# Optimization experiments

Hardware: AMD Instinct MI355X
Metric: run time of the kernel (lower is better)

Reference implementation:

```python
import jax, jax.numpy as jnp
import numpy as np

H = 256       # hidden_dim
LAT = 8       # latent_dim
NC = 8        # num_edge_classes
B = 65536     # batch of edge decisions
EPS = 1e-5    # LayerNorm eps (torch default)


def _ln(x, g, b):
    m = jnp.mean(x, axis=-1, keepdims=True)
    v = jnp.var(x, axis=-1, keepdims=True)
    return (x - m) * jax.lax.rsqrt(v + EPS) * g + b


def setup_inputs() -> dict:
    key = jax.random.key(0)
    ks = jax.random.split(key, 32)
    rn = lambda k, shape: (jax.random.normal(k, shape, dtype=jnp.float32) * 0.02)
    inp = {
        "node_i": jax.random.normal(ks[0], (B, H), dtype=jnp.float32),
        "node_j": jax.random.normal(ks[1], (B, H), dtype=jnp.float32),
        "latent": jax.random.normal(ks[2], (B, LAT), dtype=jnp.float32),
        "edge_hidden_state": jax.random.normal(ks[3], (B, H), dtype=jnp.float32),
        "previous_edge_token": jax.random.randint(ks[4], (B,), 0, NC, dtype=jnp.int32),
        # edge_encoder: Linear(2H->H) + LayerNorm
        "We": rn(ks[5], (2 * H, H)), "be": jnp.zeros((H,), jnp.float32),
        "ge": jnp.ones((H,), jnp.float32), "bee": jnp.zeros((H,), jnp.float32),
        # context_proj: Linear(LAT->H)
        "Wc": rn(ks[6], (LAT, H)), "bc": jnp.zeros((H,), jnp.float32),
        # MultiheadAttention in/out projections (q,k mathematically inert: kv_len=1)
        "Wq": rn(ks[7], (H, H)), "bq": jnp.zeros((H,), jnp.float32),
        "Wk": rn(ks[8], (H, H)), "bk": jnp.zeros((H,), jnp.float32),
        "Wv": rn(ks[9], (H, H)), "bv": jnp.zeros((H,), jnp.float32),
        "Wo": rn(ks[10], (H, H)), "bo": jnp.zeros((H,), jnp.float32),
        # post-attention LayerNorm
        "gn": jnp.ones((H,), jnp.float32), "bn": jnp.zeros((H,), jnp.float32),
        # edge token embedding [NC, H]
        "emb": rn(ks[11], (NC, H)),
        # GRUCell(2H -> H): gates packed as [r|z|n] along output dim (torch order)
        "W_ih": rn(ks[12], (2 * H, 3 * H)), "b_ih": jnp.zeros((3 * H,), jnp.float32),
        "W_hh": rn(ks[13], (H, 3 * H)), "b_hh": jnp.zeros((3 * H,), jnp.float32),
        # fusion: Linear(3H->H) + LayerNorm
        "Wf": rn(ks[14], (3 * H, H)), "bf": jnp.zeros((H,), jnp.float32),
        "gf": jnp.ones((H,), jnp.float32), "bff": jnp.zeros((H,), jnp.float32),
        # output head: Linear(H->H//2) + ReLU + Linear(H//2->NC)
        "W1": rn(ks[15], (H, H // 2)), "b1": jnp.zeros((H // 2,), jnp.float32),
        "W2": rn(ks[16], (H // 2, NC)), "b2": jnp.zeros((NC,), jnp.float32),
    }
    return inp


def _forward(node_i, node_j, latent, edge_hidden_state, previous_edge_token,
             We, be, ge, bee, Wc, bc, Wq, bq, Wk, bk, Wv, bv, Wo, bo,
             gn, bn, emb, W_ih, b_ih, W_hh, b_hh, Wf, bf, gf, bff,
             W1, b1, W2, b2):
    # edge encoder (eval mode: dropout is identity)
    edge = jax.nn.relu(_ln(jnp.concatenate([node_i, node_j], axis=-1) @ We + be, ge, bee))
    # context projection [B, H] (seq_len 1, squeezed)
    context = latent @ Wc + bc
    # cross-attention with a single key/value: softmax over one key == 1 exactly,
    # so attended = out_proj(value_proj(context)); q/k projections cancel out.
    v = context @ Wv + bv
    attended = _ln(v @ Wo + bo, gn, bn)
    prev_embed = emb[previous_edge_token]                      # [B, H]
    x = jnp.concatenate([attended, prev_embed], axis=-1)       # [B, 2H]
    gi = x @ W_ih + b_ih                                       # [B, 3H]
    gh = edge_hidden_state @ W_hh + b_hh                       # [B, 3H]
    r = jax.nn.sigmoid(gi[:, :H] + gh[:, :H])
    z = jax.nn.sigmoid(gi[:, H:2 * H] + gh[:, H:2 * H])
    n = jnp.tanh(gi[:, 2 * H:] + r * gh[:, 2 * H:])
    new_h = (1.0 - z) * n + z * edge_hidden_state
    fused = jax.nn.relu(_ln(jnp.concatenate([edge, attended, new_h], axis=-1) @ Wf + bf, gf, bff))
    logits = jax.nn.relu(fused @ W1 + b1) @ W2 + b2            # [B, NC]
    return logits, new_h


def reference(node_i, node_j, latent, edge_hidden_state, previous_edge_token,
              We, be, ge, bee, Wc, bc, Wq, bq, Wk, bk, Wv, bv, Wo, bo,
              gn, bn, emb, W_ih, b_ih, W_hh, b_hh, Wf, bf, gf, bff,
              W1, b1, W2, b2):
    return _forward(node_i, node_j, latent, edge_hidden_state, previous_edge_token,
                    We, be, ge, bee, Wc, bc, Wq, bq, Wk, bk, Wv, bv, Wo, bo,
                    gn, bn, emb, W_ih, b_ih, W_hh, b_hh, Wf, bf, gf, bff,
                    W1, b1, W2, b2)
```

## Files before the change

kernel.cpp:

```cpp
#include <hip/hip_runtime.h>


typedef __bf16 bf16;
typedef _Float16 f16;
typedef __attribute__((ext_vector_type(8))) _Float16 f16x8;
typedef __attribute__((ext_vector_type(4))) float f32x4;

#define HD 256
#define RPB 64
#define AST 260
#define AST2 264
#define TPB 1024
#define TPM 512

#define FB_OFF 65536
#define WE_E 0
#define WIH_E 131072
#define WHH_E 327680
#define WF_E 524288
#define W1_E 720896
#define FRAG_ELEMS 753664
#define WS_NEED (FB_OFF + FRAG_ELEMS * 2)

__device__ __forceinline__ float bf2f(unsigned short u) {
  union { unsigned int i; float f; } c; c.i = ((unsigned)u) << 16; return c.f;
}
__device__ __forceinline__ float4 ld4c(const float* p) { return *(const float4*)p; }
__device__ __forceinline__ float4 ld4c(const bf16* p) {
  ushort4 u = *(const ushort4*)p;
  return make_float4(bf2f(u.x), bf2f(u.y), bf2f(u.z), bf2f(u.w));
}
template <class T>
__device__ __forceinline__ float ld(const T* __restrict__ p) { return (float)*p; }

__device__ __forceinline__ f32x4 MFMA16(f16x8 a, f16x8 b, f32x4 c) {
  return __builtin_amdgcn_mfma_f32_16x16x32_f16(a, b, c, 0, 0, 0);
}

__global__ void k_detect(const unsigned int* __restrict__ wds, int* __restrict__ flag, int nw) {
  __shared__ int sRed[4];
  int t = threadIdx.x;
  int cnt = 0;
  for (int i = t; i < nw; i += 256) {
    unsigned e = (wds[i] >> 7) & 0xFFu;
    cnt += (e >= 110u && e <= 140u) ? 1 : 0;
  }
#pragma unroll
  for (int m = 1; m < 64; m <<= 1) cnt += __shfl_xor(cnt, m);
  if ((t & 63) == 0) sRed[t >> 6] = cnt;
  __syncthreads();
  if (t == 0) flag[0] = (sRed[0] + sRed[1] + sRed[2] + sRed[3] > nw / 2) ? 1 : 0;
}

template <class T, int WANT>
__global__ void k_cvo_a(const int* __restrict__ flag, const T* __restrict__ Wc,
                        const T* __restrict__ Wv, const T* __restrict__ bc,
                        const T* __restrict__ bv, float* __restrict__ tmp) {
  if (*flag != WANT) return;
  int i = blockIdx.x;
  int m = threadIdx.x;
  float s = 0.f;
  if (i < 8) {
    for (int u = 0; u < 256; ++u) s += ld(Wc + i * 256 + u) * ld(Wv + (size_t)u * 256 + m);
  } else {
    for (int u = 0; u < 256; ++u) s += ld(bc + u) * ld(Wv + (size_t)u * 256 + m);
    s += ld(bv + m);
  }
  tmp[i * 256 + m] = s;
}

template <class T, int WANT>
__global__ void k_cvo_b(const int* __restrict__ flag, const float* __restrict__ tmp,
                        const T* __restrict__ Wo, const T* __restrict__ bo,
                        float* __restrict__ Wcvo, float* __restrict__ bcvo) {
  if (*flag != WANT) return;
  int i = blockIdx.x;
  int m = threadIdx.x;
  float s = 0.f;
  const float* tr = tmp + i * 256;
  for (int u = 0; u < 256; ++u) s += tr[u] * ld(Wo + (size_t)u * 256 + m);
  if (i < 8) Wcvo[i * 256 + m] = s;
  else       bcvo[m] = s + ld(bo + m);
}

__global__ void k_prep(const int* __restrict__ flag,
                       const float* We, const float* Wih, const float* Whh,
                       const float* Wf, const float* W1, f16* __restrict__ dst) {
  if (*flag != 0) return;
  const float* srcs[5] = {We, Wih, Whh, Wf, W1};
  const int Ns[5] = {256, 768, 768, 256, 128};
  const int offs[6] = {WE_E, WIH_E, WHH_E, WF_E, W1_E, FRAG_ELEMS};
  int t = blockIdx.x * blockDim.x + threadIdx.x;
  int np = gridDim.x * blockDim.x;
  for (int seg = 0; seg < 5; ++seg) {
    const float* s = srcs[seg];
    int N = Ns[seg], NT = N >> 4;
    f16* d = dst + offs[seg];
    int n = offs[seg + 1] - offs[seg];
    for (int e = t; e < n; e += np) {
      int j = e & 7, lx = (e >> 3) & 63, tl = e >> 9;
      int kt = tl / NT, nt = tl - kt * NT;
      int sk = kt * 32 + ((lx >> 4) << 3) + j;
      int sn = nt * 16 + (lx & 15);
      d[e] = (f16)s[(size_t)sk * N + sn];
    }
  }
}

__global__ void k_egru(const int* __restrict__ flag, const float* __restrict__ emb,
                       const float* __restrict__ Wih, const float* __restrict__ b_ih,
                       float* __restrict__ E) {
  if (*flag != 0) return;
  int tok = blockIdx.x, c = threadIdx.x;
  float s = b_ih[c];
  for (int k = 0; k < 256; ++k)
    s += emb[tok * 256 + k] * Wih[(size_t)(256 + k) * 768 + c];
  E[tok * 768 + c] = s;
}

__device__ __forceinline__ void mm4(f32x4 acc[2][4], const f16* __restrict__ X,
                                    int rowBase, int ktA0, int nKt,
                                    const f16* __restrict__ WB, int NT,
                                    int ktB0, int ntB, int lane16, int lg, int l) {
#pragma unroll 2
  for (int kt = 0; kt < nKt; ++kt) {
    const f16* xp = X + (size_t)(rowBase + lane16) * AST2 + (ktA0 + kt) * 32 + lg * 8;
    f16x8 a0 = *(const f16x8*)xp;
    f16x8 a1 = *(const f16x8*)(xp + 16 * AST2);
    const f16* wp = WB + (((size_t)(ktB0 + kt) * NT + ntB) * 64 + l) * 8;
#pragma unroll
    for (int nti = 0; nti < 4; ++nti) {
      f16x8 bfr = *(const f16x8*)(wp + nti * 512);
      acc[0][nti] = MFMA16(a0, bfr, acc[0][nti]);
      acc[1][nti] = MFMA16(a1, bfr, acc[1][nti]);
    }
  }
}

__device__ __forceinline__ void mm2(f32x4 acc[2][2], const f16* __restrict__ X,
                                    int rowBase, const f16* __restrict__ WB,
                                    int ntB, int lane16, int lg, int l) {
#pragma unroll 2
  for (int kt = 0; kt < 8; ++kt) {
    const f16* xp = X + (size_t)(rowBase + lane16) * AST2 + kt * 32 + lg * 8;
    f16x8 a0 = *(const f16x8*)xp;
    f16x8 a1 = *(const f16x8*)(xp + 16 * AST2);
    const f16* wp = WB + (((size_t)kt * 8 + ntB) * 64 + l) * 8;
#pragma unroll
    for (int nti = 0; nti < 2; ++nti) {
      f16x8 bfr = *(const f16x8*)(wp + nti * 512);
      acc[0][nti] = MFMA16(a0, bfr, acc[0][nti]);
      acc[1][nti] = MFMA16(a1, bfr, acc[1][nti]);
    }
  }
}

__device__ __forceinline__ void zero4(f32x4 acc[2][4]) {
#pragma unroll
  for (int a = 0; a < 2; ++a)
#pragma unroll
    for (int b = 0; b < 4; ++b) acc[a][b] = (f32x4){0.f, 0.f, 0.f, 0.f};
}

__device__ __forceinline__ void addB4(f32x4 acc[2][4], const float* bvec, int cg, int lane16) {
#pragma unroll
  for (int nti = 0; nti < 4; ++nti) {
    float bv = bvec[(cg * 4 + nti) * 16 + lane16];
#pragma unroll
    for (int rti = 0; rti < 2; ++rti)
#pragma unroll
      for (int r = 0; r < 4; ++r) acc[rti][nti][r] += bv;
  }
}

__device__ __forceinline__ void addE4(f32x4 acc[2][4], const float* __restrict__ E768,
                                      const int* __restrict__ tokS, int gateOff,
                                      int rtp, int cg, int lane16, int lg) {
#pragma unroll
  for (int rti = 0; rti < 2; ++rti)
#pragma unroll
    for (int r = 0; r < 4; ++r) {
      int grow = (rtp * 2 + rti) * 16 + lg * 4 + r;
      const float* er = E768 + tokS[grow] * 768 + gateOff;
#pragma unroll
      for (int nti = 0; nti < 4; ++nti)
        acc[rti][nti][r] += er[(cg * 4 + nti) * 16 + lane16];
    }
}

__device__ __forceinline__ void lnD(f32x4 acc[2][4], int rtp, int cg, int lane16, int lg,
                                    float* red, const float* g, const float* b, bool relu) {
  float sv[2][4], qv[2][4];
#pragma unroll
  for (int rti = 0; rti < 2; ++rti)
#pragma unroll
    for (int r = 0; r < 4; ++r) {
      float s = 0.f, q = 0.f;
#pragma unroll
      for (int nti = 0; nti < 4; ++nti) { float v = acc[rti][nti][r]; s += v; q += v * v; }
#pragma unroll
      for (int m = 1; m < 16; m <<= 1) { s += __shfl_xor(s, m); q += __shfl_xor(q, m); }
      sv[rti][r] = s; qv[rti][r] = q;
    }
  __syncthreads();
  if (lane16 == 0) {
#pragma unroll
    for (int rti = 0; rti < 2; ++rti)
#pragma unroll
      for (int r = 0; r < 4; ++r) {
        int grow = (rtp * 2 + rti) * 16 + lg * 4 + r;
        red[grow * 8 + cg * 2] = sv[rti][r];
        red[grow * 8 + cg * 2 + 1] = qv[rti][r];
      }
  }
  __syncthreads();
  float gv[4], bv[4];
#pragma unroll
  for (int nti = 0; nti < 4; ++nti) {
    int gc = (cg * 4 + nti) * 16 + lane16;
    gv[nti] = g[gc]; bv[nti] = b[gc];
  }
#pragma unroll
  for (int rti = 0; rti < 2; ++rti)
#pragma unroll
    for (int r = 0; r < 4; ++r) {
      int grow = (rtp * 2 + rti) * 16 + lg * 4 + r;
      float s = red[grow * 8 + 0] + red[grow * 8 + 2] + red[grow * 8 + 4] + red[grow * 8 + 6];
      float q = red[grow * 8 + 1] + red[grow * 8 + 3] + red[grow * 8 + 5] + red[grow * 8 + 7];
      float mean = s * (1.f / 256.f);
      float var = q * (1.f / 256.f) - mean * mean;
      float rstd = rsqrtf(var + 1e-5f);
#pragma unroll
      for (int nti = 0; nti < 4; ++nti) {
        float v = (acc[rti][nti][r] - mean) * rstd * gv[nti] + bv[nti];
        acc[rti][nti][r] = relu ? fmaxf(v, 0.f) : v;
      }
    }
}

__device__ __forceinline__ void scatD(f16* X, const f32x4 acc[2][4], int rtp, int cg,
                                      int lane16, int lg) {
#pragma unroll
  for (int rti = 0; rti < 2; ++rti)
#pragma unroll
    for (int r = 0; r < 4; ++r) {
      int grow = (rtp * 2 + rti) * 16 + lg * 4 + r;
#pragma unroll
      for (int nti = 0; nti < 4; ++nti) {
        int gc = (cg * 4 + nti) * 16 + lane16;
        X[(size_t)grow * AST2 + gc] = (f16)acc[rti][nti][r];
      }
    }
}

__device__ __forceinline__ void stageH(f16* dst, const float* __restrict__ src,
                                       int nv, int t) {
#pragma unroll
  for (int ii = 0; ii < 4; ++ii) {
    int i = t + ii * TPM;
    int r = i >> 5, c8 = i & 31;
    f16x8 h = (f16x8)(_Float16)0;
    if (r < nv) {
      const float* p = src + (size_t)r * HD + c8 * 8;
      float4 v0 = *(const float4*)p, v1 = *(const float4*)(p + 4);
      h[0] = (f16)v0.x; h[1] = (f16)v0.y; h[2] = (f16)v0.z; h[3] = (f16)v0.w;
      h[4] = (f16)v1.x; h[5] = (f16)v1.y; h[6] = (f16)v1.z; h[7] = (f16)v1.w;
    }
    *(f16x8*)(dst + (size_t)r * AST2 + c8 * 8) = h;
  }
}

__global__ __launch_bounds__(TPM, 4) void k_mfma(
    const int* __restrict__ flag, int Brows,
    const float* __restrict__ node_i, const float* __restrict__ node_j,
    const float* __restrict__ latent, const float* __restrict__ hin,
    const int* __restrict__ tok,
    const float* __restrict__ be, const float* __restrict__ ge, const float* __restrict__ bee,
    const float* __restrict__ gn, const float* __restrict__ bn,
    const float* __restrict__ b_hh,
    const float* __restrict__ bfb, const float* __restrict__ gf, const float* __restrict__ bff,
    const float* __restrict__ b1, const float* __restrict__ W2, const float* __restrict__ b2,
    const f16* __restrict__ WeF, const f16* __restrict__ WihF,
    const f16* __restrict__ WhhF, const f16* __restrict__ WfF,
    const f16* __restrict__ W1F,
    const float* __restrict__ Wcvo, const float* __restrict__ bcvo,
    const float* __restrict__ E768,
    float* __restrict__ outL, float* __restrict__ outNH) {
  if (*flag != 0) return;
  extern __shared__ char smc[];
  f16* X1 = (f16*)smc;
  f16* X2 = (f16*)(smc + 33792);
  float* red = (float*)(smc + 67584);
  float* sc  = (float*)(smc + 71680);
  int* tokS  = (int*)(smc + 73728);

  const int t = threadIdx.x;
  const int w = __builtin_amdgcn_readfirstlane(t >> 6);
  const int l = t & 63;
  const int lane16 = l & 15, lg = l >> 4;
  const int rtp = w & 1;
  const int cg = w >> 1;
  const int rowBase = rtp * 32;
  const int row0 = blockIdx.x * RPB;
  int nv = Brows - row0; if (nv > RPB) nv = RPB;

  if (t < 64) tokS[t] = (t < nv) ? tok[row0 + t] : 0;
  if (t < 512) sc[t] = ((t >> 3) < nv) ? latent[(size_t)row0 * 8 + t] : 0.f;
  stageH(X1, node_i + (size_t)row0 * HD, nv, t);
  __syncthreads();

  f32x4 acc[2][4];
  zero4(acc);
  mm4(acc, X1, rowBase, 0, 8, WeF, 16, 0, cg * 4, lane16, lg, l);
  __syncthreads();
  stageH(X1, node_j + (size_t)row0 * HD, nv, t);
  __syncthreads();
  mm4(acc, X1, rowBase, 0, 8, WeF, 16, 8, cg * 4, lane16, lg, l);
  addB4(acc, be, cg, lane16);
  lnD(acc, rtp, cg, lane16, lg, red, ge, bee, true);
  scatD(X2, acc, rtp, cg, lane16, lg);
  __syncthreads();

  f32x4 fac[2][4];
  zero4(fac);
  mm4(fac, X2, rowBase, 0, 8, WfF, 16, 0, cg * 4, lane16, lg, l);

  {
    float a32[32];
#pragma unroll
    for (int j4 = 0; j4 < 8; ++j4) {
      float4 v = *(const float4*)(bcvo + w * 32 + j4 * 4);
      a32[j4 * 4 + 0] = v.x; a32[j4 * 4 + 1] = v.y;
      a32[j4 * 4 + 2] = v.z; a32[j4 * 4 + 3] = v.w;
    }
#pragma unroll
    for (int k = 0; k < 8; ++k) {
      float xs = sc[l * 8 + k];
      const float* wr = Wcvo + k * 256 + w * 32;
#pragma unroll
      for (int j4 = 0; j4 < 8; ++j4) {
        float4 wv = *(const float4*)(wr + j4 * 4);
        a32[j4 * 4 + 0] = fmaf(xs, wv.x, a32[j4 * 4 + 0]);
        a32[j4 * 4 + 1] = fmaf(xs, wv.y, a32[j4 * 4 + 1]);
        a32[j4 * 4 + 2] = fmaf(xs, wv.z, a32[j4 * 4 + 2]);
        a32[j4 * 4 + 3] = fmaf(xs, wv.w, a32[j4 * 4 + 3]);
      }
    }
    float s = 0.f, q = 0.f;
#pragma unroll
    for (int j = 0; j < 32; ++j) { s += a32[j]; q += a32[j] * a32[j]; }
    __syncthreads();
    red[(w * 64 + l) * 2] = s; red[(w * 64 + l) * 2 + 1] = q;
    __syncthreads();
    s = 0.f; q = 0.f;
#pragma unroll
    for (int ww = 0; ww < 8; ++ww) {
      s += red[(ww * 64 + l) * 2]; q += red[(ww * 64 + l) * 2 + 1];
    }
    float mean = s * (1.f / 256.f);
    float var = q * (1.f / 256.f) - mean * mean;
    float rstd = rsqrtf(var + 1e-5f);
#pragma unroll
    for (int j = 0; j < 32; j += 2) {
      float v0 = (a32[j] - mean) * rstd * gn[w * 32 + j] + bn[w * 32 + j];
      float v1 = (a32[j + 1] - mean) * rstd * gn[w * 32 + j + 1] + bn[w * 32 + j + 1];
      union { f16 h[2]; unsigned u; } pu;
      pu.h[0] = (f16)v0; pu.h[1] = (f16)v1;
      *(unsigned*)(X1 + (size_t)l * AST2 + w * 32 + j) = pu.u;
    }
  }
  __syncthreads();

  mm4(fac, X1, rowBase, 0, 8, WfF, 16, 8, cg * 4, lane16, lg, l);
  stageH(X2, hin + (size_t)row0 * HD, nv, t);
  __syncthreads();

  f32x4 ghn[2][4];
  zero4(ghn);
  mm4(ghn, X2, rowBase, 0, 8, WhhF, 48, 0, 32 + cg * 4, lane16, lg, l);
  addB4(ghn, b_hh + 512, cg, lane16);

  zero4(acc);
  mm4(acc, X1, rowBase, 0, 8, WihF, 48, 0, cg * 4, lane16, lg, l);
  mm4(acc, X2, rowBase, 0, 8, WhhF, 48, 0, cg * 4, lane16, lg, l);
  addE4(acc, E768, tokS, 0, rtp, cg, lane16, lg);
  addB4(acc, b_hh, cg, lane16);
#pragma unroll
  for (int a = 0; a < 2; ++a)
#pragma unroll
    for (int b = 0; b < 4; ++b)
#pragma unroll
      for (int r = 0; r < 4; ++r) {
        float rr = 1.f / (1.f + expf(-acc[a][b][r]));
        acc[a][b][r] = rr * ghn[a][b][r];
      }

  zero4(ghn);
  mm4(ghn, X1, rowBase, 0, 8, WihF, 48, 0, 32 + cg * 4, lane16, lg, l);
  addE4(ghn, E768, tokS, 512, rtp, cg, lane16, lg);
#pragma unroll
  for (int a = 0; a < 2; ++a)
#pragma unroll
    for (int b = 0; b < 4; ++b)
#pragma unroll
      for (int r = 0; r < 4; ++r)
        ghn[a][b][r] = tanhf(ghn[a][b][r] + acc[a][b][r]);

  zero4(acc);
  mm4(acc, X1, rowBase, 0, 8, WihF, 48, 0, 16 + cg * 4, lane16, lg, l);
  mm4(acc, X2, rowBase, 0, 8, WhhF, 48, 0, 16 + cg * 4, lane16, lg, l);
  addE4(acc, E768, tokS, 256, rtp, cg, lane16, lg);
  addB4(acc, b_hh + 256, cg, lane16);
#pragma unroll
  for (int a = 0; a < 2; ++a)
#pragma unroll
    for (int r = 0; r < 4; ++r) {
      int grow = (rtp * 2 + a) * 16 + lg * 4 + r;
      const float* hrow = hin + (size_t)(row0 + grow) * HD;
      bool live = grow < nv;
#pragma unroll
      for (int b = 0; b < 4; ++b) {
        int gc = (cg * 4 + b) * 16 + lane16;
        float zz = 1.f / (1.f + expf(-acc[a][b][r]));
        float hvv = live ? hrow[gc] : 0.f;
        float nh = (1.f - zz) * ghn[a][b][r] + zz * hvv;
        acc[a][b][r] = nh;
        if (live) outNH[(size_t)(row0 + grow) * HD + gc] = nh;
      }
    }
  __syncthreads();
  scatD(X1, acc, rtp, cg, lane16, lg);
  __syncthreads();

  mm4(fac, X1, rowBase, 0, 8, WfF, 16, 16, cg * 4, lane16, lg, l);
  addB4(fac, bfb, cg, lane16);
  lnD(fac, rtp, cg, lane16, lg, red, gf, bff, true);
  scatD(X2, fac, rtp, cg, lane16, lg);
  __syncthreads();

  f32x4 acc1[2][2];
#pragma unroll
  for (int a = 0; a < 2; ++a)
#pragma unroll
    for (int b = 0; b < 2; ++b) acc1[a][b] = (f32x4){0.f, 0.f, 0.f, 0.f};
  mm2(acc1, X2, rowBase, W1F, cg * 2, lane16, lg, l);
  float* H = (float*)X1;
#pragma unroll
  for (int a = 0; a < 2; ++a)
#pragma unroll
    for (int r = 0; r < 4; ++r) {
      int grow = (rtp * 2 + a) * 16 + lg * 4 + r;
#pragma unroll
      for (int b = 0; b < 2; ++b) {
        int gc1 = (cg * 2 + b) * 16 + lane16;
        H[grow * 132 + gc1] = fmaxf(acc1[a][b][r] + b1[gc1], 0.f);
      }
    }
  __syncthreads();

  {
    int rr = t & 63, ks = w * 16;
    float p[8];
#pragma unroll
    for (int o = 0; o < 8; ++o) p[o] = 0.f;
    for (int k = 0; k < 16; ++k) {
      float hv = H[rr * 132 + ks + k];
      const float* w2r = W2 + (size_t)(ks + k) * 8;
#pragma unroll
      for (int o = 0; o < 8; ++o) p[o] = fmaf(hv, w2r[o], p[o]);
    }
    float* hp = (float*)X2;
#pragma unroll
    for (int o = 0; o < 8; ++o) hp[(w * 64 + rr) * 8 + o] = p[o];
  }
  __syncthreads();
  if (t < 64 && t < nv) {
    const float* hp = (const float*)X2;
    float o8[8];
#pragma unroll
    for (int o = 0; o < 8; ++o) {
      float s = b2[o];
#pragma unroll
      for (int ww = 0; ww < 8; ++ww) s += hp[(ww * 64 + t) * 8 + o];
      o8[o] = s;
    }
    *(float4*)(outL + (size_t)(row0 + t) * 8) = make_float4(o8[0], o8[1], o8[2], o8[3]);
    *(float4*)(outL + (size_t)(row0 + t) * 8 + 4) = make_float4(o8[4], o8[5], o8[6], o8[7]);
  }
}

template <int K, int LDW, class XT, class WT>
__device__ __forceinline__ void gemm16(float* __restrict__ acc, const XT* __restrict__ x,
                                       const WT* __restrict__ wb) {
#pragma unroll 2
  for (int k = 0; k < K; k += 4) {
    float4 xv = ld4c(x + k);
#pragma unroll
    for (int kk = 0; kk < 4; ++kk) {
      float xs = (kk == 0) ? xv.x : (kk == 1) ? xv.y : (kk == 2) ? xv.z : xv.w;
      const WT* wr = wb + (size_t)(k + kk) * LDW;
#pragma unroll
      for (int j = 0; j < 4; ++j) {
        float4 wv = ld4c(wr + j * 4);
        acc[j*4+0] = fmaf(xs, wv.x, acc[j*4+0]);
        acc[j*4+1] = fmaf(xs, wv.y, acc[j*4+1]);
        acc[j*4+2] = fmaf(xs, wv.z, acc[j*4+2]);
        acc[j*4+3] = fmaf(xs, wv.w, acc[j*4+3]);
      }
    }
  }
}

template <int K, int LDW, class XT, class WT>
__device__ __forceinline__ void gemm8(float* __restrict__ acc, const XT* __restrict__ x,
                                      const WT* __restrict__ wb) {
#pragma unroll 2
  for (int k = 0; k < K; k += 4) {
    float4 xv = ld4c(x + k);
#pragma unroll
    for (int kk = 0; kk < 4; ++kk) {
      float xs = (kk == 0) ? xv.x : (kk == 1) ? xv.y : (kk == 2) ? xv.z : xv.w;
      const WT* wr = wb + (size_t)(k + kk) * LDW;
#pragma unroll
      for (int j = 0; j < 2; ++j) {
        float4 wv = ld4c(wr + j * 4);
        acc[j*4+0] = fmaf(xs, wv.x, acc[j*4+0]);
        acc[j*4+1] = fmaf(xs, wv.y, acc[j*4+1]);
        acc[j*4+2] = fmaf(xs, wv.z, acc[j*4+2]);
        acc[j*4+3] = fmaf(xs, wv.w, acc[j*4+3]);
      }
    }
  }
}

template <class WT>
__device__ __forceinline__ void ld16v(float* d, const WT* p) {
#pragma unroll
  for (int j = 0; j < 4; ++j) {
    float4 v = ld4c(p + j * 4);
    d[j*4+0] = v.x; d[j*4+1] = v.y; d[j*4+2] = v.z; d[j*4+3] = v.w;
  }
}
template <class WT>
__device__ __forceinline__ void add16v(float* d, const WT* p) {
#pragma unroll
  for (int j = 0; j < 4; ++j) {
    float4 v = ld4c(p + j * 4);
    d[j*4+0] += v.x; d[j*4+1] += v.y; d[j*4+2] += v.z; d[j*4+3] += v.w;
  }
}
__device__ __forceinline__ void st16v(float* p, const float* a) {
#pragma unroll
  for (int j = 0; j < 4; ++j)
    *(float4*)(p + j * 4) = make_float4(a[j*4+0], a[j*4+1], a[j*4+2], a[j*4+3]);
}

template <bool RELU, class WT>
__device__ __forceinline__ void ln_apply16(float* acc, float mean, float rstd,
                                           const WT* g, const WT* b) {
#pragma unroll
  for (int j = 0; j < 4; ++j) {
    float4 gv = ld4c(g + j * 4), bv = ld4c(b + j * 4);
    acc[j*4+0] = (acc[j*4+0] - mean) * rstd * gv.x + bv.x;
    acc[j*4+1] = (acc[j*4+1] - mean) * rstd * gv.y + bv.y;
    acc[j*4+2] = (acc[j*4+2] - mean) * rstd * gv.z + bv.z;
    acc[j*4+3] = (acc[j*4+3] - mean) * rstd * gv.w + bv.w;
    if (RELU) {
      acc[j*4+0] = fmaxf(acc[j*4+0], 0.f);
      acc[j*4+1] = fmaxf(acc[j*4+1], 0.f);
      acc[j*4+2] = fmaxf(acc[j*4+2], 0.f);
      acc[j*4+3] = fmaxf(acc[j*4+3], 0.f);
    }
  }
}

__device__ __forceinline__ void ln_stats16(const float* acc, int w, int l, float* red,
                                           float& mean, float& rstd) {
  float s = 0.f, q = 0.f;
#pragma unroll
  for (int j = 0; j < 16; ++j) { s += acc[j]; q += acc[j] * acc[j]; }
  __syncthreads();
  *(float2*)(red + (w * 64 + l) * 2) = make_float2(s, q);
  __syncthreads();
  s = 0.f; q = 0.f;
#pragma unroll
  for (int ww = 0; ww < 16; ++ww) {
    float2 v = *(const float2*)(red + (ww * 64 + l) * 2);
    s += v.x; q += v.y;
  }
  mean = s * (1.f / 256.f);
  float var = q * (1.f / 256.f) - mean * mean;
  rstd = rsqrtf(var + 1e-5f);
}

template <class T>
__device__ __forceinline__ void stage256(float* dst, const T* __restrict__ src, int nv, int t) {
#pragma unroll
  for (int ii = 0; ii < 4; ++ii) {
    int i = t + ii * TPB;
    int r = i >> 6, c4 = i & 63;
    float4 v = make_float4(0.f, 0.f, 0.f, 0.f);
    if (r < nv) v = ld4c(src + (size_t)r * HD + c4 * 4);
    *(float4*)(dst + r * AST + c4 * 4) = v;
  }
}

template <class T, class WT, int WANT>
__global__ __launch_bounds__(TPB, 4) void k_row(
    const int* __restrict__ flag, int Brows,
    const T* __restrict__ node_i, const T* __restrict__ node_j,
    const T* __restrict__ latent, const T* __restrict__ hin,
    const int* __restrict__ tok,
    const WT* __restrict__ We, const WT* __restrict__ be,
    const WT* __restrict__ ge, const WT* __restrict__ bee,
    const WT* __restrict__ gn, const WT* __restrict__ bn,
    const WT* __restrict__ emb,
    const WT* __restrict__ W_ih, const WT* __restrict__ b_ih,
    const WT* __restrict__ W_hh, const WT* __restrict__ b_hh,
    const WT* __restrict__ Wf, const WT* __restrict__ bfb,
    const WT* __restrict__ gf, const WT* __restrict__ bff,
    const WT* __restrict__ W1, const WT* __restrict__ b1,
    const WT* __restrict__ W2, const WT* __restrict__ b2,
    const float* __restrict__ Wcvo, const float* __restrict__ bcvo,
    T* __restrict__ outL, T* __restrict__ outNH) {
  if (*flag != WANT) return;
  extern __shared__ float sm[];
  float* A   = sm;
  float* Bb  = sm + 64 * AST;
  float* red = sm + 2 * 64 * AST;
  float* sc  = red + 2048;
  int* tokS  = (int*)(sc + 512);

  const int t = threadIdx.x;
  const int w = __builtin_amdgcn_readfirstlane(t >> 6);
  const int l = t & 63;
  const int row0 = blockIdx.x * RPB;
  int nv = Brows - row0; if (nv > RPB) nv = RPB;
  const int cb = w * 16;

  if (t < 64) tokS[t] = (t < nv) ? tok[row0 + t] : 0;
  stage256(A, node_i + (size_t)row0 * HD, nv, t);
  __syncthreads();

  float acc[16];
  ld16v(acc, be + cb);
  gemm16<256, 256>(acc, A + l * AST, We + cb);
  __syncthreads();
  stage256(A, node_j + (size_t)row0 * HD, nv, t);
  __syncthreads();
  gemm16<256, 256>(acc, A + l * AST, We + (size_t)256 * 256 + cb);
  float mean, rstd;
  ln_stats16(acc, w, l, red, mean, rstd);
  ln_apply16<true>(acc, mean, rstd, ge + cb, bee + cb);
  st16v(Bb + l * AST + cb, acc);
  __syncthreads();

  float fac[16];
  ld16v(fac, bfb + cb);
  gemm16<256, 256>(fac, Bb + l * AST, Wf + cb);

  if (t < 512) {
    int r = t >> 3;
    sc[t] = (r < nv) ? ld(latent + (size_t)row0 * 8 + t) : 0.f;
  }
  __syncthreads();
  ld16v(acc, bcvo + cb);
  gemm16<8, 256>(acc, sc + l * 8, Wcvo + cb);
  ln_stats16(acc, w, l, red, mean, rstd);
  ln_apply16<false>(acc, mean, rstd, gn + cb, bn + cb);
  st16v(A + l * AST + cb, acc);
  __syncthreads();

  gemm16<256, 256>(fac, A + l * AST, Wf + (size_t)256 * 256 + cb);
  stage256(Bb, hin + (size_t)row0 * HD, nv, t);
  __syncthreads();

  const int tk = tokS[l];
  const WT* embr = emb + (size_t)tk * HD;

  ld16v(acc, b_ih + cb); add16v(acc, b_hh + cb);
  gemm16<256, 768>(acc, A + l * AST, W_ih + cb);
  gemm16<256, 768>(acc, embr, W_ih + (size_t)256 * 768 + cb);
  gemm16<256, 768>(acc, Bb + l * AST, W_hh + cb);
  float rg[16];
#pragma unroll
  for (int j = 0; j < 16; ++j) rg[j] = 1.f / (1.f + expf(-acc[j]));

  ld16v(acc, b_hh + 512 + cb);
  gemm16<256, 768>(acc, Bb + l * AST, W_hh + 512 + cb);
#pragma unroll
  for (int j = 0; j < 16; ++j) rg[j] *= acc[j];

  ld16v(acc, b_ih + 512 + cb);
  gemm16<256, 768>(acc, A + l * AST, W_ih + 512 + cb);
  gemm16<256, 768>(acc, embr, W_ih + (size_t)256 * 768 + 512 + cb);
#pragma unroll
  for (int j = 0; j < 16; ++j) rg[j] = tanhf(acc[j] + rg[j]);

  ld16v(acc, b_ih + 256 + cb); add16v(acc, b_hh + 256 + cb);
  gemm16<256, 768>(acc, A + l * AST, W_ih + 256 + cb);
  gemm16<256, 768>(acc, embr, W_ih + (size_t)256 * 768 + 256 + cb);
  gemm16<256, 768>(acc, Bb + l * AST, W_hh + 256 + cb);
  __syncthreads();
#pragma unroll
  for (int j4 = 0; j4 < 4; ++j4) {
    float4 hv = ld4c(Bb + l * AST + cb + j4 * 4);
    float z0 = 1.f / (1.f + expf(-acc[j4*4+0]));
    float z1 = 1.f / (1.f + expf(-acc[j4*4+1]));
    float z2 = 1.f / (1.f + expf(-acc[j4*4+2]));
    float z3 = 1.f / (1.f + expf(-acc[j4*4+3]));
    acc[j4*4+0] = (1.f - z0) * rg[j4*4+0] + z0 * hv.x;
    acc[j4*4+1] = (1.f - z1) * rg[j4*4+1] + z1 * hv.y;
    acc[j4*4+2] = (1.f - z2) * rg[j4*4+2] + z2 * hv.z;
    acc[j4*4+3] = (1.f - z3) * rg[j4*4+3] + z3 * hv.w;
  }
  st16v(Bb + l * AST + cb, acc);
  __syncthreads();

  for (int i = t; i < nv * HD; i += TPB) {
    int r = i >> 8, c = i & 255;
    outNH[(size_t)(row0 + r) * HD + c] = (T)Bb[r * AST + c];
  }

  gemm16<256, 256>(fac, Bb + l * AST, Wf + (size_t)512 * 256 + cb);
  ln_stats16(fac, w, l, red, mean, rstd);
  ln_apply16<true>(fac, mean, rstd, gf + cb, bff + cb);
  st16v(A + l * AST + cb, fac);
  __syncthreads();

  float h1[8];
  {
    float4 v0 = ld4c(b1 + w * 8), v1 = ld4c(b1 + w * 8 + 4);
    h1[0]=v0.x; h1[1]=v0.y; h1[2]=v0.z; h1[3]=v0.w;
    h1[4]=v1.x; h1[5]=v1.y; h1[6]=v1.z; h1[7]=v1.w;
  }
  gemm8<256, 128>(h1, A + l * AST, W1 + w * 8);
  float part[8];
#pragma unroll
  for (int o = 0; o < 8; ++o) part[o] = 0.f;
#pragma unroll
  for (int kk = 0; kk < 8; ++kk) {
    float hval = fmaxf(h1[kk], 0.f);
    const WT* w2r = W2 + (size_t)(w * 8 + kk) * 8;
    float4 a0 = ld4c(w2r), a1 = ld4c(w2r + 4);
    part[0] = fmaf(hval, a0.x, part[0]);
    part[1] = fmaf(hval, a0.y, part[1]);
    part[2] = fmaf(hval, a0.z, part[2]);
    part[3] = fmaf(hval, a0.w, part[3]);
    part[4] = fmaf(hval, a1.x, part[4]);
    part[5] = fmaf(hval, a1.y, part[5]);
    part[6] = fmaf(hval, a1.z, part[6]);
    part[7] = fmaf(hval, a1.w, part[7]);
  }
  float* hp = Bb;
  *(float4*)(hp + (w * 64 + l) * 8)     = make_float4(part[0], part[1], part[2], part[3]);
  *(float4*)(hp + (w * 64 + l) * 8 + 4) = make_float4(part[4], part[5], part[6], part[7]);
  __syncthreads();
  if (w == 0 && l < nv) {
#pragma unroll
    for (int o = 0; o < 8; ++o) {
      float lg = ld(b2 + o);
#pragma unroll
      for (int ww = 0; ww < 16; ++ww) lg += hp[(ww * 64 + l) * 8 + o];
      outL[(size_t)(row0 + l) * 8 + o] = (T)lg;
    }
  }
}

extern "C" void kernel_launch(void* const* d_in, const int* in_sizes, int n_in,
                              void* d_out, int out_size, void* d_ws, size_t ws_size,
                              hipStream_t stream) {
  char* ws = (char*)d_ws;
  const int B = in_sizes[0] / HD;
  const int nblk = (B + RPB - 1) / RPB;
  int* flag = (int*)ws;
  float* tmpcv = (float*)(ws + 1024);
  float* Wcvo  = (float*)(ws + 16384);
  float* bcvo  = (float*)(ws + 24576);
  float* E768  = (float*)(ws + 28672);
  f16*   fragW = (f16*)(ws + FB_OFF);

  int nw = B * 128; if (nw > 16384) nw = 16384;
  k_detect<<<1, 256, 0, stream>>>((const unsigned int*)d_in[0], flag, nw);

  const size_t SMEM_F = (size_t)(2 * 64 * AST + 2048 + 512) * 4 + 64 * 4;
  const size_t SMEM_M = 73984;

  {
    auto P = [&](int i) { return (const float*)d_in[i]; };
    k_cvo_a<float, 0><<<9, 256, 0, stream>>>(flag, P(9), P(15), P(10), P(16), tmpcv);
    k_cvo_b<float, 0><<<9, 256, 0, stream>>>(flag, tmpcv, P(17), P(18), Wcvo, bcvo);
    if (ws_size >= (size_t)WS_NEED) {
      k_prep<<<512, 256, 0, stream>>>(flag, P(5), P(22), P(24), P(26), P(30), fragW);
      k_egru<<<8, 768, 0, stream>>>(flag, P(21), P(22), P(23), E768);
      (void)hipFuncSetAttribute(reinterpret_cast<const void*>(&k_mfma),
                                hipFuncAttributeMaxDynamicSharedMemorySize, (int)SMEM_M);
      k_mfma<<<nblk, TPM, SMEM_M, stream>>>(
          flag, B, P(0), P(1), P(2), P(3), (const int*)d_in[4],
          P(6), P(7), P(8),
          P(19), P(20),
          P(25),
          P(27), P(28), P(29),
          P(31), P(32), P(33),
          fragW + WE_E, fragW + WIH_E, fragW + WHH_E, fragW + WF_E, fragW + W1_E,
          Wcvo, bcvo, E768,
          (float*)d_out, (float*)d_out + (size_t)B * 8);
    } else {
      (void)hipFuncSetAttribute(reinterpret_cast<const void*>(&k_row<float, float, 0>),
                                hipFuncAttributeMaxDynamicSharedMemorySize, (int)SMEM_F);
      k_row<float, float, 0><<<nblk, TPB, SMEM_F, stream>>>(
          flag, B, P(0), P(1), P(2), P(3), (const int*)d_in[4],
          P(5), P(6), P(7), P(8), P(19), P(20), P(21),
          P(22), P(23), P(24), P(25), P(26), P(27), P(28), P(29),
          P(30), P(31), P(32), P(33), Wcvo, bcvo,
          (float*)d_out, (float*)d_out + (size_t)B * 8);
    }
  }
  {
    auto P = [&](int i) { return (const bf16*)d_in[i]; };
    k_cvo_a<bf16, 1><<<9, 256, 0, stream>>>(flag, P(9), P(15), P(10), P(16), tmpcv);
    k_cvo_b<bf16, 1><<<9, 256, 0, stream>>>(flag, tmpcv, P(17), P(18), Wcvo, bcvo);
    bf16* oL = (bf16*)d_out;
    (void)hipFuncSetAttribute(reinterpret_cast<const void*>(&k_row<bf16, bf16, 1>),
                              hipFuncAttributeMaxDynamicSharedMemorySize, (int)SMEM_F);
    k_row<bf16, bf16, 1><<<nblk, TPB, SMEM_F, stream>>>(
        flag, B, P(0), P(1), P(2), P(3), (const int*)d_in[4],
        P(5), P(6), P(7), P(8), P(19), P(20), P(21),
        P(22), P(23), P(24), P(25), P(26), P(27), P(28), P(29),
        P(30), P(31), P(32), P(33), Wcvo, bcvo, oL, oL + (size_t)B * 8);
  }
}
```

Before: 666.6 us.

## Merge prep kernels into one launch and split GRU gate computation into halves

Merges the weight-fragment prep, embedding-GRU table, and context/value/output folding into a single k_pre1 launch plus a k_pre2 launch, cutting the number of small preprocessing launches. In the MFMA kernel, the GRU gates are computed in two halves of two column tiles each, which lowers live accumulator registers. The new hidden state is read straight back from the global output, converting to f16 on the fly, for the fusion matmul instead of being scattered to shared memory. This trades a shared-memory round trip and one barrier for extra global reads, and redoes the A-fragment loads once per half.

```diff
diff --git a/kernel.cpp b/kernel.cpp
--- a/kernel.cpp
+++ b/kernel.cpp
@@ -52,79 +52,92 @@
   if (t == 0) flag[0] = (sRed[0] + sRed[1] + sRed[2] + sRed[3] > nw / 2) ? 1 : 0;
 }
 
-template <class T, int WANT>
-__global__ void k_cvo_a(const int* __restrict__ flag, const T* __restrict__ Wc,
-                        const T* __restrict__ Wv, const T* __restrict__ bc,
-                        const T* __restrict__ bv, float* __restrict__ tmp) {
-  if (*flag != WANT) return;
-  int i = blockIdx.x;
-  int m = threadIdx.x;
-  float s = 0.f;
-  if (i < 8) {
-    for (int u = 0; u < 256; ++u) s += ld(Wc + i * 256 + u) * ld(Wv + (size_t)u * 256 + m);
+__global__ void k_pre1(const int* __restrict__ flag, int doPrep,
+                       const void* We, const void* Wih, const void* Whh,
+                       const void* Wf, const void* W1,
+                       const void* emb, const void* b_ih,
+                       const void* Wc, const void* Wv, const void* bc, const void* bv,
+                       f16* __restrict__ fragW, float* __restrict__ E768,
+                       float* __restrict__ tmp) {
+  const int fl = *flag;
+  const int bid = blockIdx.x, t = threadIdx.x;
+  if (bid < 512) {
+    if (fl != 0 || !doPrep) return;
+    const float* srcs[5] = {(const float*)We, (const float*)Wih, (const float*)Whh,
+                            (const float*)Wf, (const float*)W1};
+    const int Ns[5] = {256, 768, 768, 256, 128};
+    const int offs[6] = {WE_E, WIH_E, WHH_E, WF_E, W1_E, FRAG_ELEMS};
+    int g = bid * 256 + t, np = 512 * 256;
+    for (int seg = 0; seg < 5; ++seg) {
+      const float* s = srcs[seg];
+      int N = Ns[seg], NT = N >> 4;
+      f16* d = fragW + offs[seg];
+      int n = offs[seg + 1] - offs[seg];
+      for (int e = g; e < n; e += np) {
+        int j = e & 7, lx = (e >> 3) & 63, tl = e >> 9;
+        int kt = tl / NT, nt = tl - kt * NT;
+        int sk = kt * 32 + ((lx >> 4) << 3) + j;
+        int sn = nt * 16 + (lx & 15);
+        d[e] = (f16)s[(size_t)sk * N + sn];
+      }
+    }
+  } else if (bid < 520) {
+    if (fl != 0 || !doPrep) return;
+    int tok = bid - 512;
+    const float* E = (const float*)emb;
+    const float* W = (const float*)Wih;
+    const float* B = (const float*)b_ih;
+    for (int c = t; c < 768; c += 256) {
+      float s = B[c];
+      for (int k = 0; k < 256; ++k)
+        s += E[tok * 256 + k] * W[(size_t)(256 + k) * 768 + c];
+      E768[tok * 768 + c] = s;
+    }
   } else {
-    for (int u = 0; u < 256; ++u) s += ld(bc + u) * ld(Wv + (size_t)u * 256 + m);
-    s += ld(bv + m);
-  }
-  tmp[i * 256 + m] = s;
-}
-
-template <class T, int WANT>
-__global__ void k_cvo_b(const int* __restrict__ flag, const float* __restrict__ tmp,
-                        const T* __restrict__ Wo, const T* __restrict__ bo,
-                        float* __restrict__ Wcvo, float* __restrict__ bcvo) {
-  if (*flag != WANT) return;
-  int i = blockIdx.x;
-  int m = threadIdx.x;
+    int i = bid - 520;
+    int m = t;
+    float s = 0.f;
+    if (fl == 0) {
+      const float* wc = (const float*)Wc; const float* wv = (const float*)Wv;
+      const float* pc = (const float*)bc; const float* pv = (const float*)bv;
+      if (i < 8) { for (int u = 0; u < 256; ++u) s += wc[i * 256 + u] * wv[(size_t)u * 256 + m]; }
+      else { for (int u = 0; u < 256; ++u) s += pc[u] * wv[(size_t)u * 256 + m]; s += pv[m]; }
+    } else {
+      const bf16* wc = (const bf16*)Wc; const bf16* wv = (const bf16*)Wv;
+      const bf16* pc = (const bf16*)bc; const bf16* pv = (const bf16*)bv;
+      if (i < 8) { for (int u = 0; u < 256; ++u) s += ld(wc + i * 256 + u) * ld(wv + (size_t)u * 256 + m); }
+      else { for (int u = 0; u < 256; ++u) s += ld(pc + u) * ld(wv + (size_t)u * 256 + m); s += ld(pv + m); }
+    }
+    tmp[i * 256 + m] = s;
+  }
+}
+
+__global__ void k_pre2(const int* __restrict__ flag, const float* __restrict__ tmp,
+                       const void* Wo, const void* bo,
+                       float* __restrict__ Wcvo, float* __restrict__ bcvo) {
+  const int fl = *flag;
+  int i = blockIdx.x, m = threadIdx.x;
   float s = 0.f;
   const float* tr = tmp + i * 256;
-  for (int u = 0; u < 256; ++u) s += tr[u] * ld(Wo + (size_t)u * 256 + m);
-  if (i < 8) Wcvo[i * 256 + m] = s;
-  else       bcvo[m] = s + ld(bo + m);
-}
-
-__global__ void k_prep(const int* __restrict__ flag,
-                       const float* We, const float* Wih, const float* Whh,
-                       const float* Wf, const float* W1, f16* __restrict__ dst) {
-  if (*flag != 0) return;
-  const float* srcs[5] = {We, Wih, Whh, Wf, W1};
-  const int Ns[5] = {256, 768, 768, 256, 128};
-  const int offs[6] = {WE_E, WIH_E, WHH_E, WF_E, W1_E, FRAG_ELEMS};
-  int t = blockIdx.x * blockDim.x + threadIdx.x;
-  int np = gridDim.x * blockDim.x;
-  for (int seg = 0; seg < 5; ++seg) {
-    const float* s = srcs[seg];
-    int N = Ns[seg], NT = N >> 4;
-    f16* d = dst + offs[seg];
-    int n = offs[seg + 1] - offs[seg];
-    for (int e = t; e < n; e += np) {
-      int j = e & 7, lx = (e >> 3) & 63, tl = e >> 9;
-      int kt = tl / NT, nt = tl - kt * NT;
-      int sk = kt * 32 + ((lx >> 4) << 3) + j;
-      int sn = nt * 16 + (lx & 15);
-      d[e] = (f16)s[(size_t)sk * N + sn];
-    }
-  }
-}
-
-__global__ void k_egru(const int* __restrict__ flag, const float* __restrict__ emb,
-                       const float* __restrict__ Wih, const float* __restrict__ b_ih,
-                       float* __restrict__ E) {
-  if (*flag != 0) return;
-  int tok = blockIdx.x, c = threadIdx.x;
-  float s = b_ih[c];
-  for (int k = 0; k < 256; ++k)
-    s += emb[tok * 256 + k] * Wih[(size_t)(256 + k) * 768 + c];
-  E[tok * 768 + c] = s;
+  if (fl == 0) {
+    const float* wo = (const float*)Wo;
+    for (int u = 0; u < 256; ++u) s += tr[u] * wo[(size_t)u * 256 + m];
+    if (i < 8) Wcvo[i * 256 + m] = s;
+    else       bcvo[m] = s + ((const float*)bo)[m];
+  } else {
+    const bf16* wo = (const bf16*)Wo;
+    for (int u = 0; u < 256; ++u) s += tr[u] * ld(wo + (size_t)u * 256 + m);
+    if (i < 8) Wcvo[i * 256 + m] = s;
+    else       bcvo[m] = s + ld((const bf16*)bo + m);
+  }
 }
 
 __device__ __forceinline__ void mm4(f32x4 acc[2][4], const f16* __restrict__ X,
-                                    int rowBase, int ktA0, int nKt,
-                                    const f16* __restrict__ WB, int NT,
+                                    int rowBase, const f16* __restrict__ WB, int NT,
                                     int ktB0, int ntB, int lane16, int lg, int l) {
 #pragma unroll 2
-  for (int kt = 0; kt < nKt; ++kt) {
-    const f16* xp = X + (size_t)(rowBase + lane16) * AST2 + (ktA0 + kt) * 32 + lg * 8;
+  for (int kt = 0; kt < 8; ++kt) {
+    const f16* xp = X + (size_t)(rowBase + lane16) * AST2 + kt * 32 + lg * 8;
     f16x8 a0 = *(const f16x8*)xp;
     f16x8 a1 = *(const f16x8*)(xp + 16 * AST2);
     const f16* wp = WB + (((size_t)(ktB0 + kt) * NT + ntB) * 64 + l) * 8;
@@ -137,15 +150,15 @@
   }
 }
 
-__device__ __forceinline__ void mm2(f32x4 acc[2][2], const f16* __restrict__ X,
-                                    int rowBase, const f16* __restrict__ WB,
+__device__ __forceinline__ void mmh(f32x4 acc[2][2], const f16* __restrict__ X,
+                                    int rowBase, const f16* __restrict__ WB, int NT,
                                     int ntB, int lane16, int lg, int l) {
 #pragma unroll 2
   for (int kt = 0; kt < 8; ++kt) {
     const f16* xp = X + (size_t)(rowBase + lane16) * AST2 + kt * 32 + lg * 8;
     f16x8 a0 = *(const f16x8*)xp;
     f16x8 a1 = *(const f16x8*)(xp + 16 * AST2);
-    const f16* wp = WB + (((size_t)kt * 8 + ntB) * 64 + l) * 8;
+    const f16* wp = WB + (((size_t)kt * NT + ntB) * 64 + l) * 8;
 #pragma unroll
     for (int nti = 0; nti < 2; ++nti) {
       f16x8 bfr = *(const f16x8*)(wp + nti * 512);
@@ -155,11 +168,42 @@
   }
 }
 
+__device__ __forceinline__ void mm4g(f32x4 acc[2][4], const float* __restrict__ Xg,
+                                     int rowBase, const f16* __restrict__ WB, int NT,
+                                     int ktB0, int ntB, int lane16, int lg, int l) {
+#pragma unroll 2
+  for (int kt = 0; kt < 8; ++kt) {
+    const float* xp = Xg + (size_t)(rowBase + lane16) * HD + kt * 32 + lg * 8;
+    float4 u0 = *(const float4*)xp, u1 = *(const float4*)(xp + 4);
+    f16x8 a0;
+    a0[0] = (f16)u0.x; a0[1] = (f16)u0.y; a0[2] = (f16)u0.z; a0[3] = (f16)u0.w;
+    a0[4] = (f16)u1.x; a0[5] = (f16)u1.y; a0[6] = (f16)u1.z; a0[7] = (f16)u1.w;
+    const float* yp = xp + 16 * HD;
+    float4 v0 = *(const float4*)yp, v1 = *(const float4*)(yp + 4);
+    f16x8 a1;
+    a1[0] = (f16)v0.x; a1[1] = (f16)v0.y; a1[2] = (f16)v0.z; a1[3] = (f16)v0.w;
+    a1[4] = (f16)v1.x; a1[5] = (f16)v1.y; a1[6] = (f16)v1.z; a1[7] = (f16)v1.w;
+    const f16* wp = WB + (((size_t)(ktB0 + kt) * NT + ntB) * 64 + l) * 8;
+#pragma unroll
+    for (int nti = 0; nti < 4; ++nti) {
+      f16x8 bfr = *(const f16x8*)(wp + nti * 512);
+      acc[0][nti] = MFMA16(a0, bfr, acc[0][nti]);
+      acc[1][nti] = MFMA16(a1, bfr, acc[1][nti]);
+    }
+  }
+}
+
 __device__ __forceinline__ void zero4(f32x4 acc[2][4]) {
 #pragma unroll
   for (int a = 0; a < 2; ++a)
 #pragma unroll
     for (int b = 0; b < 4; ++b) acc[a][b] = (f32x4){0.f, 0.f, 0.f, 0.f};
+}
+__device__ __forceinline__ void zero2(f32x4 acc[2][2]) {
+#pragma unroll
+  for (int a = 0; a < 2; ++a)
+#pragma unroll
+    for (int b = 0; b < 2; ++b) acc[a][b] = (f32x4){0.f, 0.f, 0.f, 0.f};
 }
 
 __device__ __forceinline__ void addB4(f32x4 acc[2][4], const float* bvec, int cg, int lane16) {
@@ -172,10 +216,19 @@
       for (int r = 0; r < 4; ++r) acc[rti][nti][r] += bv;
   }
 }
-
-__device__ __forceinline__ void addE4(f32x4 acc[2][4], const float* __restrict__ E768,
+__device__ __forceinline__ void addB2(f32x4 acc[2][2], const float* bvec, int ntB, int lane16) {
+#pragma unroll
+  for (int nti = 0; nti < 2; ++nti) {
+    float bv = bvec[(ntB + nti) * 16 + lane16];
+#pragma unroll
+    for (int rti = 0; rti < 2; ++rti)
+#pragma unroll
+      for (int r = 0; r < 4; ++r) acc[rti][nti][r] += bv;
+  }
+}
+__device__ __forceinline__ void addE2(f32x4 acc[2][2], const float* __restrict__ E768,
                                       const int* __restrict__ tokS, int gateOff,
-                                      int rtp, int cg, int lane16, int lg) {
+                                      int rtp, int ntB, int lane16, int lg) {
 #pragma unroll
   for (int rti = 0; rti < 2; ++rti)
 #pragma unroll
@@ -183,8 +236,8 @@
       int grow = (rtp * 2 + rti) * 16 + lg * 4 + r;
       const float* er = E768 + tokS[grow] * 768 + gateOff;
 #pragma unroll
-      for (int nti = 0; nti < 4; ++nti)
-        acc[rti][nti][r] += er[(cg * 4 + nti) * 16 + lane16];
+      for (int nti = 0; nti < 2; ++nti)
+        acc[rti][nti][r] += er[(ntB + nti) * 16 + lane16];
     }
 }
 
@@ -311,11 +364,11 @@
 
   f32x4 acc[2][4];
   zero4(acc);
-  mm4(acc, X1, rowBase, 0, 8, WeF, 16, 0, cg * 4, lane16, lg, l);
+  mm4(acc, X1, rowBase, WeF, 16, 0, cg * 4, lane16, lg, l);
   __syncthreads();
   stageH(X1, node_j + (size_t)row0 * HD, nv, t);
   __syncthreads();
-  mm4(acc, X1, rowBase, 0, 8, WeF, 16, 8, cg * 4, lane16, lg, l);
+  mm4(acc, X1, rowBase, WeF, 16, 8, cg * 4, lane16, lg, l);
   addB4(acc, be, cg, lane16);
   lnD(acc, rtp, cg, lane16, lg, red, ge, bee, true);
   scatD(X2, acc, rtp, cg, lane16, lg);
@@ -323,7 +376,7 @@
 
   f32x4 fac[2][4];
   zero4(fac);
-  mm4(fac, X2, rowBase, 0, 8, WfF, 16, 0, cg * 4, lane16, lg, l);
+  mm4(fac, X2, rowBase, WfF, 16, 0, cg * 4, lane16, lg, l);
 
   {
     float a32[32];
@@ -371,79 +424,78 @@
   }
   __syncthreads();
 
-  mm4(fac, X1, rowBase, 0, 8, WfF, 16, 8, cg * 4, lane16, lg, l);
+  mm4(fac, X1, rowBase, WfF, 16, 8, cg * 4, lane16, lg, l);
   stageH(X2, hin + (size_t)row0 * HD, nv, t);
   __syncthreads();
 
-  f32x4 ghn[2][4];
-  zero4(ghn);
-  mm4(ghn, X2, rowBase, 0, 8, WhhF, 48, 0, 32 + cg * 4, lane16, lg, l);
-  addB4(ghn, b_hh + 512, cg, lane16);
-
-  zero4(acc);
-  mm4(acc, X1, rowBase, 0, 8, WihF, 48, 0, cg * 4, lane16, lg, l);
-  mm4(acc, X2, rowBase, 0, 8, WhhF, 48, 0, cg * 4, lane16, lg, l);
-  addE4(acc, E768, tokS, 0, rtp, cg, lane16, lg);
-  addB4(acc, b_hh, cg, lane16);
-#pragma unroll
-  for (int a = 0; a < 2; ++a)
-#pragma unroll
-    for (int b = 0; b < 4; ++b)
+#pragma unroll
+  for (int h = 0; h < 2; ++h) {
+    const int ntB = cg * 4 + h * 2;
+    f32x4 ghn[2][2];
+    zero2(ghn);
+    mmh(ghn, X2, rowBase, WhhF, 48, 32 + ntB, lane16, lg, l);
+    addB2(ghn, b_hh + 512, ntB, lane16);
+
+    f32x4 g2[2][2];
+    zero2(g2);
+    mmh(g2, X1, rowBase, WihF, 48, ntB, lane16, lg, l);
+    mmh(g2, X2, rowBase, WhhF, 48, ntB, lane16, lg, l);
+    addE2(g2, E768, tokS, 0, rtp, ntB, lane16, lg);
+    addB2(g2, b_hh, ntB, lane16);
+#pragma unroll
+    for (int a = 0; a < 2; ++a)
+#pragma unroll
+      for (int b = 0; b < 2; ++b)
+#pragma unroll
+        for (int r = 0; r < 4; ++r) {
+          float rr = 1.f / (1.f + expf(-g2[a][b][r]));
+          ghn[a][b][r] *= rr;
+        }
+
+    zero2(g2);
+    mmh(g2, X1, rowBase, WihF, 48, 32 + ntB, lane16, lg, l);
+    addE2(g2, E768, tokS, 512, rtp, ntB, lane16, lg);
+#pragma unroll
+    for (int a = 0; a < 2; ++a)
+#pragma unroll
+      for (int b = 0; b < 2; ++b)
+#pragma unroll
+        for (int r = 0; r < 4; ++r)
+          ghn[a][b][r] = tanhf(g2[a][b][r] + ghn[a][b][r]);
+
+    zero2(g2);
+    mmh(g2, X1, rowBase, WihF, 48, 16 + ntB, lane16, lg, l);
+    mmh(g2, X2, rowBase, WhhF, 48, 16 + ntB, lane16, lg, l);
+    addE2(g2, E768, tokS, 256, rtp, ntB, lane16, lg);
+    addB2(g2, b_hh + 256, ntB, lane16);
+#pragma unroll
+    for (int a = 0; a < 2; ++a)
 #pragma unroll
       for (int r = 0; r < 4; ++r) {
-        float rr = 1.f / (1.f + expf(-acc[a][b][r]));
-        acc[a][b][r] = rr * ghn[a][b][r];
+        int grow = (rtp * 2 + a) * 16 + lg * 4 + r;
+        bool live = grow < nv;
+        float* orow = outNH + (size_t)(row0 + grow) * HD;
+#pragma unroll
+        for (int b = 0; b < 2; ++b) {
+          int gc = (ntB + b) * 16 + lane16;
+          float zz = 1.f / (1.f + expf(-g2[a][b][r]));
+          float hv = (float)X2[(size_t)grow * AST2 + gc];
+          float nh = (1.f - zz) * ghn[a][b][r] + zz * hv;
+          if (live) orow[gc] = nh;
+        }
       }
-
-  zero4(ghn);
-  mm4(ghn, X1, rowBase, 0, 8, WihF, 48, 0, 32 + cg * 4, lane16, lg, l);
-  addE4(ghn, E768, tokS, 512, rtp, cg, lane16, lg);
-#pragma unroll
-  for (int a = 0; a < 2; ++a)
-#pragma unroll
-    for (int b = 0; b < 4; ++b)
-#pragma unroll
-      for (int r = 0; r < 4; ++r)
-        ghn[a][b][r] = tanhf(ghn[a][b][r] + acc[a][b][r]);
-
-  zero4(acc);
-  mm4(acc, X1, rowBase, 0, 8, WihF, 48, 0, 16 + cg * 4, lane16, lg, l);
-  mm4(acc, X2, rowBase, 0, 8, WhhF, 48, 0, 16 + cg * 4, lane16, lg, l);
-  addE4(acc, E768, tokS, 256, rtp, cg, lane16, lg);
-  addB4(acc, b_hh + 256, cg, lane16);
-#pragma unroll
-  for (int a = 0; a < 2; ++a)
-#pragma unroll
-    for (int r = 0; r < 4; ++r) {
-      int grow = (rtp * 2 + a) * 16 + lg * 4 + r;
-      const float* hrow = hin + (size_t)(row0 + grow) * HD;
-      bool live = grow < nv;
-#pragma unroll
-      for (int b = 0; b < 4; ++b) {
-        int gc = (cg * 4 + b) * 16 + lane16;
-        float zz = 1.f / (1.f + expf(-acc[a][b][r]));
-        float hvv = live ? hrow[gc] : 0.f;
-        float nh = (1.f - zz) * ghn[a][b][r] + zz * hvv;
-        acc[a][b][r] = nh;
-        if (live) outNH[(size_t)(row0 + grow) * HD + gc] = nh;
-      }
-    }
-  __syncthreads();
-  scatD(X1, acc, rtp, cg, lane16, lg);
-  __syncthreads();
-
-  mm4(fac, X1, rowBase, 0, 8, WfF, 16, 16, cg * 4, lane16, lg, l);
+  }
+  __syncthreads();
+
+  mm4g(fac, outNH + (size_t)row0 * HD, rowBase, WfF, 16, 16, cg * 4, lane16, lg, l);
   addB4(fac, bfb, cg, lane16);
   lnD(fac, rtp, cg, lane16, lg, red, gf, bff, true);
   scatD(X2, fac, rtp, cg, lane16, lg);
   __syncthreads();
 
   f32x4 acc1[2][2];
-#pragma unroll
-  for (int a = 0; a < 2; ++a)
-#pragma unroll
-    for (int b = 0; b < 2; ++b) acc1[a][b] = (f32x4){0.f, 0.f, 0.f, 0.f};
-  mm2(acc1, X2, rowBase, W1F, cg * 2, lane16, lg, l);
+  zero2(acc1);
+  mmh(acc1, X2, rowBase, W1F, 8, cg * 2, lane16, lg, l);
   float* H = (float*)X1;
 #pragma unroll
   for (int a = 0; a < 2; ++a)
@@ -779,20 +831,24 @@
   float* bcvo  = (float*)(ws + 24576);
   float* E768  = (float*)(ws + 28672);
   f16*   fragW = (f16*)(ws + FB_OFF);
+  const int doPrep = (ws_size >= (size_t)WS_NEED) ? 1 : 0;
 
   int nw = B * 128; if (nw > 16384) nw = 16384;
   k_detect<<<1, 256, 0, stream>>>((const unsigned int*)d_in[0], flag, nw);
 
+  k_pre1<<<529, 256, 0, stream>>>(flag, doPrep,
+      d_in[5], d_in[22], d_in[24], d_in[26], d_in[30],
+      d_in[21], d_in[23],
+      d_in[9], d_in[15], d_in[10], d_in[16],
+      fragW, E768, tmpcv);
+  k_pre2<<<9, 256, 0, stream>>>(flag, tmpcv, d_in[17], d_in[18], Wcvo, bcvo);
+
   const size_t SMEM_F = (size_t)(2 * 64 * AST + 2048 + 512) * 4 + 64 * 4;
   const size_t SMEM_M = 73984;
 
   {
     auto P = [&](int i) { return (const float*)d_in[i]; };
-    k_cvo_a<float, 0><<<9, 256, 0, stream>>>(flag, P(9), P(15), P(10), P(16), tmpcv);
-    k_cvo_b<float, 0><<<9, 256, 0, stream>>>(flag, tmpcv, P(17), P(18), Wcvo, bcvo);
-    if (ws_size >= (size_t)WS_NEED) {
-      k_prep<<<512, 256, 0, stream>>>(flag, P(5), P(22), P(24), P(26), P(30), fragW);
-      k_egru<<<8, 768, 0, stream>>>(flag, P(21), P(22), P(23), E768);
+    if (doPrep) {
       (void)hipFuncSetAttribute(reinterpret_cast<const void*>(&k_mfma),
                                 hipFuncAttributeMaxDynamicSharedMemorySize, (int)SMEM_M);
       k_mfma<<<nblk, TPM, SMEM_M, stream>>>(
@@ -818,8 +874,6 @@
   }
   {
     auto P = [&](int i) { return (const bf16*)d_in[i]; };
-    k_cvo_a<bf16, 1><<<9, 256, 0, stream>>>(flag, P(9), P(15), P(10), P(16), tmpcv);
-    k_cvo_b<bf16, 1><<<9, 256, 0, stream>>>(flag, tmpcv, P(17), P(18), Wcvo, bcvo);
     bf16* oL = (bf16*)d_out;
     (void)hipFuncSetAttribute(reinterpret_cast<const void*>(&k_row<bf16, bf16, 1>),
                               hipFuncAttributeMaxDynamicSharedMemorySize, (int)SMEM_F);
```

Result: faster. 617.1 us (-7.4%).
